# Kernel optimization log

Hardware: AMD Instinct MI355X
Metric: run time of the kernel (lower is better)

Reference implementation:

```python
import jax, jax.numpy as jnp
import numpy as np

EMBED_DIM = 1024
NUM_HEADS = 16
HEAD_DIM = EMBED_DIM // NUM_HEADS
FF_DIM = 4096
EPS = 1e-5


def layer_norm(x, gamma, beta):
    mu = jnp.mean(x, axis=-1, keepdims=True)
    var = jnp.var(x, axis=-1, keepdims=True)
    return (x - mu) * jax.lax.rsqrt(var + EPS) * gamma + beta


def setup_inputs() -> dict:
    key = jax.random.key(0)
    ks = jax.random.split(key, 10)
    B, S = 2, 2048
    sd = 1.0 / np.sqrt(EMBED_DIM)
    sf = 1.0 / np.sqrt(FF_DIM)
    return {
        "x": jax.random.normal(ks[0], (B, S, EMBED_DIM), jnp.float32),
        # grouped QKV: 3*num_heads groups, each embed_dim -> head_dim
        "Wqkv": jax.random.normal(ks[1], (3 * NUM_HEADS, EMBED_DIM, HEAD_DIM), jnp.float32) * sd,
        "bqkv": jnp.zeros((3 * NUM_HEADS, HEAD_DIM), jnp.float32),
        "Wo": jax.random.normal(ks[2], (EMBED_DIM, EMBED_DIM), jnp.float32) * sd,
        "bo": jnp.zeros((EMBED_DIM,), jnp.float32),
        "W1": jax.random.normal(ks[3], (EMBED_DIM, FF_DIM), jnp.float32) * sd,
        "b1": jnp.zeros((FF_DIM,), jnp.float32),
        "W2": jax.random.normal(ks[4], (FF_DIM, EMBED_DIM), jnp.float32) * sf,
        "b2": jnp.zeros((EMBED_DIM,), jnp.float32),
        "ln1_g": jnp.ones((EMBED_DIM,), jnp.float32),
        "ln1_b": jnp.zeros((EMBED_DIM,), jnp.float32),
        "ln2_g": jnp.ones((EMBED_DIM,), jnp.float32),
        "ln2_b": jnp.zeros((EMBED_DIM,), jnp.float32),
    }


def reference(x, Wqkv, bqkv, Wo, bo, W1, b1, W2, b2, ln1_g, ln1_b, ln2_g, ln2_b):
    B, S, D = x.shape
    normed = layer_norm(x, ln1_g, ln1_b)
    # grouped QKV projection: group g gets its own (D, head_dim) weight
    qkv = jnp.einsum('bsd,gdh->bgsh', normed, Wqkv) + bqkv[None, :, None, :]
    qkv = qkv.reshape(B, 3, NUM_HEADS, S, HEAD_DIM)
    q, k, v = qkv[:, 0], qkv[:, 1], qkv[:, 2]  # each [B, H, S, hd]
    attn = jnp.einsum('bhqd,bhkd->bhqk', q, k) / np.sqrt(HEAD_DIM)
    attn = jax.nn.softmax(attn, axis=-1)
    out = jnp.einsum('bhqk,bhkd->bhqd', attn, v)
    out = out.transpose(0, 2, 1, 3).reshape(B, S, D)
    out = out @ Wo + bo
    x = x + out
    normed2 = layer_norm(x, ln2_g, ln2_b)
    ff = jax.nn.relu(normed2 @ W1 + b1) @ W2 + b2
    return x + ff
```

## Files before the change

kernel.cpp:

```cpp
#include <hip/hip_runtime.h>
#include <stdint.h>

#define SEQ    2048
#define NB     2
#define NHEADS 16
#define HDIM   64
#define EMBED  1024
#define NROWS  (NB*SEQ)
#define QKVSZ  ((size_t)NB*NHEADS*SEQ*HDIM)

typedef __attribute__((ext_vector_type(8))) short short8;
typedef __attribute__((ext_vector_type(4))) float float4v;
typedef __attribute__((ext_vector_type(16))) float float16v;
typedef __attribute__((ext_vector_type(2))) unsigned int uint2v;
typedef __attribute__((ext_vector_type(4))) unsigned int uint4v;

__device__ __forceinline__ float b2f(unsigned short h) {
    unsigned int u = ((unsigned int)h) << 16;
    union { unsigned int u; float f; } c; c.u = u; return c.f;
}
__device__ __forceinline__ unsigned short f2b(float f) {
    union { float f; unsigned int u; } c; c.f = f;
    unsigned int u = c.u;
    u += 0x7FFFu + ((u >> 16) & 1u);
    return (unsigned short)(u >> 16);
}
__device__ __forceinline__ unsigned int fbits(float f) {
    union { float f; unsigned int u; } c; c.f = f; return c.u;
}
__device__ __forceinline__ unsigned int cvtpk_bf16(float lo, float hi) {
    unsigned int r;
    asm("v_cvt_pk_bf16_f32 %0, %1, %2" : "=v"(r) : "v"(lo), "v"(hi));
    return r;
}

__device__ __forceinline__ void gload_lds16(const void* g, void* l) {
    __builtin_amdgcn_global_load_lds(
        (const __attribute__((address_space(1))) unsigned int*)g,
        (__attribute__((address_space(3))) unsigned int*)l, 16, 0, 0);
}

__device__ __forceinline__ int probe_f32(const void* probe) {
    return ((const unsigned short*)probe)[0] == 0;
}
__device__ __forceinline__ float lde(const void* base, size_t off, int f32) {
    return f32 ? ((const float*)base)[off] : b2f(((const unsigned short*)base)[off]);
}
__device__ __forceinline__ void ste(void* base, size_t off, float v, int f32) {
    if (f32) ((float*)base)[off] = v;
    else     ((unsigned short*)base)[off] = f2b(v);
}

__global__ __launch_bounds__(256) void ln_kernel(
    const void* __restrict__ x,
    const void* __restrict__ g,
    const void* __restrict__ b,
    unsigned short* __restrict__ out,
    const void* __restrict__ probe)
{
    int f32 = probe_f32(probe);
    int row = blockIdx.x;
    int t = threadIdx.x;
    float v0, v1, v2, v3;
    if (f32) {
        float4 rv = ((const float4*)x)[(size_t)row * (EMBED / 4) + t];
        v0 = rv.x; v1 = rv.y; v2 = rv.z; v3 = rv.w;
    } else {
        ushort4 rv = ((const ushort4*)((const unsigned short*)x + (size_t)row * EMBED))[t];
        v0 = b2f(rv.x); v1 = b2f(rv.y); v2 = b2f(rv.z); v3 = b2f(rv.w);
    }
    float s  = v0 + v1 + v2 + v3;
    float sq = v0*v0 + v1*v1 + v2*v2 + v3*v3;
    #pragma unroll
    for (int off = 32; off > 0; off >>= 1) {
        s  += __shfl_xor(s,  off);
        sq += __shfl_xor(sq, off);
    }
    __shared__ float red[8];
    int lane = t & 63, wv = t >> 6;
    if (lane == 0) { red[wv] = s; red[wv + 4] = sq; }
    __syncthreads();
    s  = red[0] + red[1] + red[2] + red[3];
    sq = red[4] + red[5] + red[6] + red[7];
    float mu  = s * (1.0f / EMBED);
    float var = sq * (1.0f / EMBED) - mu * mu;
    float rs  = rsqrtf(var + 1e-5f);
    float g0 = lde(g, t*4+0, f32), g1 = lde(g, t*4+1, f32);
    float g2 = lde(g, t*4+2, f32), g3 = lde(g, t*4+3, f32);
    float b0 = lde(b, t*4+0, f32), b1 = lde(b, t*4+1, f32);
    float b2 = lde(b, t*4+2, f32), b3 = lde(b, t*4+3, f32);
    ushort4 ov;
    ov.x = f2b((v0 - mu) * rs * g0 + b0);
    ov.y = f2b((v1 - mu) * rs * g1 + b1);
    ov.z = f2b((v2 - mu) * rs * g2 + b2);
    ov.w = f2b((v3 - mu) * rs * g3 + b3);
    ((ushort4*)(out + (size_t)row * EMBED))[t] = ov;
}

template<int QKV>
__global__ __launch_bounds__(256) void transpose_kernel(
    const void* __restrict__ in,
    unsigned short* __restrict__ out, int K, int N,
    const void* __restrict__ probe)
{
    __shared__ unsigned short t[64 * 68];
    int f32 = probe_f32(probe);
    int tid = threadIdx.x;
    int n0 = blockIdx.x * 64, k0 = blockIdx.y * 64;
    #pragma unroll
    for (int i = 0; i < 4; i++) {
        int id = tid + i * 256;
        int kr = id >> 4, nc = (id & 15) * 4;
        size_t srcoff;
        if (QKV) srcoff = ((size_t)(n0 >> 6) << 16) + (size_t)(k0 + kr) * 64 + nc;
        else     srcoff = (size_t)(k0 + kr) * N + n0 + nc;
        ushort4 val;
        if (f32) {
            float4 rv = *(const float4*)((const float*)in + srcoff);
            val.x = f2b(rv.x); val.y = f2b(rv.y); val.z = f2b(rv.z); val.w = f2b(rv.w);
        } else {
            val = *(const ushort4*)((const unsigned short*)in + srcoff);
        }
        *(ushort4*)&t[kr * 68 + nc] = val;
    }
    __syncthreads();
    #pragma unroll
    for (int i = 0; i < 4; i++) {
        int id = tid + i * 256;
        int nr = id >> 4, kc = (id & 15) * 4;
        ushort4 o;
        o.x = t[(kc + 0) * 68 + nr];
        o.y = t[(kc + 1) * 68 + nr];
        o.z = t[(kc + 2) * 68 + nr];
        o.w = t[(kc + 3) * 68 + nr];
        *(ushort4*)(out + (size_t)(n0 + nr) * K + k0 + kc) = o;
    }
}

template<int DO_RELU, int HAS_BIAS, int OUTMODE>
__global__ __launch_bounds__(512) void gemm256_kernel(
    const unsigned short* __restrict__ A,
    const unsigned short* __restrict__ Bt,
    const void* __restrict__ bias,
    void* __restrict__ out,
    int M, int N, int Kloc, int ldA, int ldB,
    const void* __restrict__ probe)
{
    __shared__ unsigned short Als[2][256 * 64];
    __shared__ unsigned short Bls[2][256 * 64];
    int f32 = probe_f32(probe);
    int tid = threadIdx.x;
    int lane = tid & 63, wv = tid >> 6;
    int lq = lane >> 4, lr = lane & 15;
    int wr = wv >> 2, wc = wv & 3;
    int m0 = blockIdx.y * 256, n0 = blockIdx.x * 256;
    int k0 = blockIdx.z * Kloc;

    int srow = tid >> 3;
    int sch  = (tid & 7) ^ (srow & 7);
    const unsigned short* ga = A  + (size_t)(m0 + srow) * ldA + k0 + sch * 8;
    const unsigned short* gb = Bt + (size_t)(n0 + srow) * ldB + k0 + sch * 8;
    int ldst = tid * 8;
    int rx = lr & 7;

    float4v acc[8][4];
    #pragma unroll
    for (int i = 0; i < 8; i++)
        #pragma unroll
        for (int j = 0; j < 4; j++)
            { acc[i][j][0] = 0.f; acc[i][j][1] = 0.f; acc[i][j][2] = 0.f; acc[i][j][3] = 0.f; }

    int nkt = Kloc >> 6;
    #pragma unroll
    for (int u = 0; u < 4; u++)
        gload_lds16(ga + (size_t)u * 64 * ldA, &Als[0][u * 4096 + ldst]);
    #pragma unroll
    for (int u = 0; u < 4; u++)
        gload_lds16(gb + (size_t)u * 64 * ldB, &Bls[0][u * 4096 + ldst]);

    for (int kt = 0; kt < nkt; kt++) {
        int cur = kt & 1, nxt = cur ^ 1;
        if (kt + 1 < nkt) {
            int ko = (kt + 1) * 64;
            #pragma unroll
            for (int u = 0; u < 4; u++)
                gload_lds16(ga + (size_t)u * 64 * ldA + ko, &Als[nxt][u * 4096 + ldst]);
            asm volatile("s_waitcnt vmcnt(4)" ::: "memory");
        } else {
            asm volatile("s_waitcnt vmcnt(0)" ::: "memory");
        }
        __builtin_amdgcn_s_barrier();
        asm volatile("" ::: "memory");
        {
            short8 af[8], bf[4];
            #pragma unroll
            for (int mt = 0; mt < 8; mt++)
                af[mt] = *(const short8*)(
                    &Als[cur][(wr * 128 + mt * 16 + lr) * 64 + ((lq ^ rx) * 8)]);
            #pragma unroll
            for (int nt = 0; nt < 4; nt++)
                bf[nt] = *(const short8*)(
                    &Bls[cur][(wc * 64 + nt * 16 + lr) * 64 + ((lq ^ rx) * 8)]);
            __builtin_amdgcn_s_setprio(1);
            #pragma unroll
            for (int mt = 0; mt < 8; mt++)
                #pragma unroll
                for (int nt = 0; nt < 4; nt++)
                    acc[mt][nt] = __builtin_amdgcn_mfma_f32_16x16x32_bf16(af[mt], bf[nt], acc[mt][nt], 0, 0, 0);
            __builtin_amdgcn_s_setprio(0);
        }
        if (kt + 1 < nkt) {
            int ko = (kt + 1) * 64;
            #pragma unroll
            for (int u = 0; u < 4; u++)
                gload_lds16(gb + (size_t)u * 64 * ldB + ko, &Bls[nxt][u * 4096 + ldst]);
        }
        {
            short8 af[8], bf[4];
            #pragma unroll
            for (int mt = 0; mt < 8; mt++)
                af[mt] = *(const short8*)(
                    &Als[cur][(wr * 128 + mt * 16 + lr) * 64 + (((4 + lq) ^ rx) * 8)]);
            #pragma unroll
            for (int nt = 0; nt < 4; nt++)
                bf[nt] = *(const short8*)(
                    &Bls[cur][(wc * 64 + nt * 16 + lr) * 64 + (((4 + lq) ^ rx) * 8)]);
            __builtin_amdgcn_s_setprio(1);
            #pragma unroll
            for (int mt = 0; mt < 8; mt++)
                #pragma unroll
                for (int nt = 0; nt < 4; nt++)
                    acc[mt][nt] = __builtin_amdgcn_mfma_f32_16x16x32_bf16(af[mt], bf[nt], acc[mt][nt], 0, 0, 0);
            __builtin_amdgcn_s_setprio(0);
        }
        asm volatile("s_waitcnt lgkmcnt(0)" ::: "memory");
        __builtin_amdgcn_s_barrier();
    }

    if (OUTMODE == 3) {
        float* po = (float*)out + (size_t)blockIdx.z * M * N;
        #pragma unroll
        for (int mt = 0; mt < 8; mt++)
            #pragma unroll
            for (int nt = 0; nt < 4; nt++)
                #pragma unroll
                for (int rg = 0; rg < 4; rg++) {
                    int rr = m0 + wr * 128 + mt * 16 + lq * 4 + rg;
                    int cc = n0 + wc * 64 + nt * 16 + lr;
                    po[(size_t)rr * N + cc] = acc[mt][nt][rg];
                }
    } else if (OUTMODE == 2) {
        #pragma unroll
        for (int mt = 0; mt < 8; mt++) {
            int rrb = m0 + wr * 128 + mt * 16 + lq * 4;
            int bb = rrb >> 11, ss = rrb & 2047;
            #pragma unroll
            for (int nt = 0; nt < 4; nt++) {
                int cc = n0 + wc * 64 + nt * 16 + lr;
                int gg = cc >> 6, hd = cc & 63;
                int ty = gg >> 4, hh = gg & 15;
                float vv[4];
                #pragma unroll
                for (int rg = 0; rg < 4; rg++) {
                    float v = acc[mt][nt][rg];
                    if (HAS_BIAS) v += lde(bias, (size_t)cc, f32);
                    vv[rg] = v;
                }
                if (ty < 2) {
                    unsigned short* p = (unsigned short*)out + (size_t)ty * QKVSZ +
                        (((size_t)(bb * NHEADS + hh) * SEQ + ss) * HDIM) + hd;
                    #pragma unroll
                    for (int rg = 0; rg < 4; rg++) p[(size_t)rg * HDIM] = f2b(vv[rg]);
                } else {
                    ushort4 pk;
                    pk.x = f2b(vv[0]); pk.y = f2b(vv[1]);
                    pk.z = f2b(vv[2]); pk.w = f2b(vv[3]);
                    *(ushort4*)((unsigned short*)out + 2 * QKVSZ +
                        ((size_t)(bb * NHEADS + hh) * HDIM + hd) * SEQ + ss) = pk;
                }
            }
        }
    } else {
        #pragma unroll
        for (int mt = 0; mt < 8; mt++)
            #pragma unroll
            for (int nt = 0; nt < 4; nt++)
                #pragma unroll
                for (int rg = 0; rg < 4; rg++) {
                    int rr = m0 + wr * 128 + mt * 16 + lq * 4 + rg;
                    int cc = n0 + wc * 64 + nt * 16 + lr;
                    float v = acc[mt][nt][rg];
                    if (HAS_BIAS) v += lde(bias, (size_t)cc, f32);
                    if (DO_RELU) v = v > 0.f ? v : 0.f;
                    ((unsigned short*)out)[(size_t)rr * N + cc] = f2b(v);
                }
    }
}

template<int DO_RELU, int HAS_BIAS, int OUTMODE>
__global__ __launch_bounds__(512) void gemm256p8_kernel(
    const unsigned short* __restrict__ A,
    const unsigned short* __restrict__ Bt,
    const void* __restrict__ bias,
    void* __restrict__ out,
    int M, int N, int Kloc, int ldA, int ldB,
    const void* __restrict__ probe)
{
    __shared__ unsigned short Als[2][2][128 * 64];
    __shared__ unsigned short Bls[2][2][128 * 64];
    int f32 = probe_f32(probe);
    int tid = threadIdx.x;
    int lane = tid & 63, wv = tid >> 6;
    int lq = lane >> 4, lr = lane & 15;
    int wr = wv >> 2, wc = wv & 3;
    int m0 = blockIdx.y * 256, n0 = blockIdx.x * 256;
    int k0 = blockIdx.z * Kloc;

    int srow = tid >> 3;
    int sch  = (tid & 7) ^ (srow & 7);
    const unsigned short* ga = A  + (size_t)(m0 + srow) * ldA + k0 + sch * 8;
    const unsigned short* gb = Bt + (size_t)(n0 + srow) * ldB + k0 + sch * 8;
    int ldst = tid * 8;
    int rx = lr & 7;

    auto stA = [&](int d, int h, int ko) {
        gload_lds16(ga + (size_t)(h * 128) * ldA + ko, &Als[d][h][ldst]);
        gload_lds16(ga + (size_t)(h * 128 + 64) * ldA + ko, &Als[d][h][4096 + ldst]);
    };
    auto stB = [&](int d, int h, int ko) {
        gload_lds16(gb + (size_t)(h * 128) * ldB + ko, &Bls[d][h][ldst]);
        gload_lds16(gb + (size_t)(h * 128 + 64) * ldB + ko, &Bls[d][h][4096 + ldst]);
    };
    auto rdA = [&](int d, int qm, short8 (&af)[4][2]) {
        #pragma unroll
        for (int mt = 0; mt < 4; mt++)
            #pragma unroll
            for (int c = 0; c < 2; c++)
                af[mt][c] = *(const short8*)(&Als[d][qm][
                    (wr * 64 + mt * 16 + lr) * 64 + (((c * 4 + lq) ^ rx) * 8)]);
    };
    auto rdB = [&](int d, int qn, short8 (&bf)[2][2]) {
        #pragma unroll
        for (int nt = 0; nt < 2; nt++)
            #pragma unroll
            for (int c = 0; c < 2; c++)
                bf[nt][c] = *(const short8*)(&Bls[d][qn][
                    (wc * 32 + nt * 16 + lr) * 64 + (((c * 4 + lq) ^ rx) * 8)]);
    };
    auto MM = [&](short8 (&af)[4][2], short8 (&bf)[2][2], float4v (&aq)[4][2]) {
        __builtin_amdgcn_s_setprio(1);
        #pragma unroll
        for (int c = 0; c < 2; c++)
            #pragma unroll
            for (int mt = 0; mt < 4; mt++)
                #pragma unroll
                for (int nt = 0; nt < 2; nt++)
                    aq[mt][nt] = __builtin_amdgcn_mfma_f32_16x16x32_bf16(
                        af[mt][c], bf[nt][c], aq[mt][nt], 0, 0, 0);
        __builtin_amdgcn_s_setprio(0);
    };
    #define VMC(n)  asm volatile("s_waitcnt vmcnt(" #n ")" ::: "memory")
    #define BARF()  do { __builtin_amdgcn_s_barrier(); \
                         asm volatile("" ::: "memory"); } while (0)

    float4v acc00[4][2], acc01[4][2], acc11[4][2], acc10[4][2];
    #pragma unroll
    for (int i = 0; i < 4; i++)
        #pragma unroll
        for (int j = 0; j < 2; j++) {
            acc00[i][j] = float4v{0.f, 0.f, 0.f, 0.f};
            acc01[i][j] = float4v{0.f, 0.f, 0.f, 0.f};
            acc11[i][j] = float4v{0.f, 0.f, 0.f, 0.f};
            acc10[i][j] = float4v{0.f, 0.f, 0.f, 0.f};
        }
    short8 af0[4][2], af1[4][2], bf0[2][2], bf1[2][2];

    int nkt = Kloc >> 6;
    int npair = nkt >> 1;

    stA(0, 0, 0); stB(0, 0, 0); stB(0, 1, 0); stA(0, 1, 0);
    VMC(4); BARF();
    rdA(0, 0, af0); rdB(0, 0, bf0);

    for (int p = 0; p < npair - 1; p++) {
        int koB  = (2 * p + 1) * 64;
        int koA2 = (2 * p + 2) * 64;
        MM(af0, bf0, acc00); stA(1, 0, koB); VMC(4); BARF(); rdB(0, 1, bf1);
        MM(af0, bf1, acc01); stB(1, 0, koB); VMC(4); BARF(); rdA(0, 1, af1);
        MM(af1, bf1, acc11); stB(1, 1, koB);         BARF(); rdB(0, 0, bf0);
        MM(af1, bf0, acc10); stA(1, 1, koB); VMC(4); BARF(); rdA(1, 0, af0); rdB(1, 0, bf1);
        MM(af0, bf1, acc00); stA(0, 0, koA2); VMC(4); BARF(); rdB(1, 1, bf0);
        MM(af0, bf0, acc01); stB(0, 0, koA2); VMC(4); BARF(); rdA(1, 1, af1);
        MM(af1, bf0, acc11); stB(0, 1, koA2);         BARF(); rdB(1, 0, bf1);
        MM(af1, bf1, acc10); stA(0, 1, koA2); VMC(4); BARF(); rdA(0, 0, af0); rdB(0, 0, bf0);
    }
    {
        int koB = (nkt - 1) * 64;
        MM(af0, bf0, acc00); stA(1, 0, koB); VMC(4); BARF(); rdB(0, 1, bf1);
        MM(af0, bf1, acc01); stB(1, 0, koB); VMC(4); BARF(); rdA(0, 1, af1);
        MM(af1, bf1, acc11); stB(1, 1, koB);         BARF(); rdB(0, 0, bf0);
        MM(af1, bf0, acc10); stA(1, 1, koB); VMC(4); BARF(); rdA(1, 0, af0); rdB(1, 0, bf1);
        MM(af0, bf1, acc00);                  VMC(2); BARF(); rdB(1, 1, bf0);
        MM(af0, bf0, acc01);                  VMC(0); BARF(); rdA(1, 1, af1);
        MM(af1, bf0, acc11);                          BARF(); rdB(1, 0, bf1);
        MM(af1, bf1, acc10);
    }
    #undef VMC
    #undef BARF

    auto storeQ = [&](int qr, int qc, float4v (&aq)[4][2]) {
        if (OUTMODE == 3) {
            float* po = (float*)out + (size_t)blockIdx.z * M * N;
            #pragma unroll
            for (int mt = 0; mt < 4; mt++)
                #pragma unroll
                for (int nt = 0; nt < 2; nt++)
                    #pragma unroll
                    for (int rg = 0; rg < 4; rg++) {
                        int rr = m0 + qr * 128 + wr * 64 + mt * 16 + lq * 4 + rg;
                        int cc = n0 + qc * 128 + wc * 32 + nt * 16 + lr;
                        po[(size_t)rr * N + cc] = aq[mt][nt][rg];
                    }
        } else {
            #pragma unroll
            for (int mt = 0; mt < 4; mt++)
                #pragma unroll
                for (int nt = 0; nt < 2; nt++)
                    #pragma unroll
                    for (int rg = 0; rg < 4; rg++) {
                        int rr = m0 + qr * 128 + wr * 64 + mt * 16 + lq * 4 + rg;
                        int cc = n0 + qc * 128 + wc * 32 + nt * 16 + lr;
                        float v = aq[mt][nt][rg];
                        if (HAS_BIAS) v += lde(bias, (size_t)cc, f32);
                        if (DO_RELU) v = v > 0.f ? v : 0.f;
                        ((unsigned short*)out)[(size_t)rr * N + cc] = f2b(v);
                    }
        }
    };
    storeQ(0, 0, acc00); storeQ(0, 1, acc01);
    storeQ(1, 1, acc11); storeQ(1, 0, acc10);
}

__global__ __launch_bounds__(256) void ff2_combine_kernel(
    const float* __restrict__ part,
    const void* __restrict__ b2,
    void* __restrict__ xout,
    const void* __restrict__ probe)
{
    int f32 = probe_f32(probe);
    int row = blockIdx.x;
    int t = threadIdx.x;
    const size_t MN = (size_t)NROWS * EMBED;
    size_t base = (size_t)row * EMBED + t * 4;
    float4 p0 = *(const float4*)(part + base);
    float4 p1 = *(const float4*)(part + MN + base);
    float4 p2 = *(const float4*)(part + 2 * MN + base);
    float4 p3 = *(const float4*)(part + 3 * MN + base);
    float s0 = (p0.x + p1.x) + (p2.x + p3.x);
    float s1 = (p0.y + p1.y) + (p2.y + p3.y);
    float s2 = (p0.z + p1.z) + (p2.z + p3.z);
    float s3 = (p0.w + p1.w) + (p2.w + p3.w);
    int c = t * 4;
    s0 += lde(b2, c + 0, f32) + lde(xout, base + 0, f32);
    s1 += lde(b2, c + 1, f32) + lde(xout, base + 1, f32);
    s2 += lde(b2, c + 2, f32) + lde(xout, base + 2, f32);
    s3 += lde(b2, c + 3, f32) + lde(xout, base + 3, f32);
    ste(xout, base + 0, s0, f32);
    ste(xout, base + 1, s1, f32);
    ste(xout, base + 2, s2, f32);
    ste(xout, base + 3, s3, f32);
}

template<int DO_RELU, int HAS_BIAS, int HAS_RES, int OUTMODE>
__global__ __launch_bounds__(256) void gemm64_kernel(
    const unsigned short* __restrict__ A,
    const unsigned short* __restrict__ Bt,
    const void* __restrict__ bias,
    const void* __restrict__ res,
    void* __restrict__ out,
    int M, int N, int K, int ldA, int ldB,
    const void* __restrict__ probe)
{
    __shared__ unsigned short Als[2][64 * 32];
    __shared__ unsigned short Bls[2][64 * 32];
    int f32 = probe_f32(probe);
    int tid = threadIdx.x;
    int lane = tid & 63, wv = tid >> 6;
    int lq = lane >> 4, lr = lane & 15;
    int moff = (wv >> 1) * 32, noff = (wv & 1) * 32;
    int m0 = blockIdx.y * 64, n0 = blockIdx.x * 64;

    int rA = tid >> 2, jA = tid & 3;
    int jjA = jA ^ ((rA >> 1) & 3);
    const unsigned short* ga = A  + (size_t)(m0 + rA) * ldA + jjA * 8;
    const unsigned short* gb = Bt + (size_t)(n0 + rA) * ldB + jjA * 8;

    int fch = (lq ^ ((lr >> 1) & 3)) * 8;

    float4v acc[2][2];
    #pragma unroll
    for (int i = 0; i < 2; i++)
        #pragma unroll
        for (int j = 0; j < 2; j++)
            { acc[i][j][0] = 0.f; acc[i][j][1] = 0.f; acc[i][j][2] = 0.f; acc[i][j][3] = 0.f; }

    gload_lds16(ga, &Als[0][(size_t)tid * 8]);
    gload_lds16(gb, &Bls[0][(size_t)tid * 8]);

    int nkt = K >> 5;
    for (int kt = 0; kt < nkt; kt++) {
        int cur = kt & 1, nxt = cur ^ 1;
        __syncthreads();
        if (kt + 1 < nkt) {
            int ko = (kt + 1) * 32;
            gload_lds16(ga + ko, &Als[nxt][(size_t)tid * 8]);
            gload_lds16(gb + ko, &Bls[nxt][(size_t)tid * 8]);
        }
        short8 af[2], bfr[2];
        #pragma unroll
        for (int mt = 0; mt < 2; mt++)
            af[mt] = *(const short8*)(&Als[cur][(moff + mt * 16 + lr) * 32 + fch]);
        #pragma unroll
        for (int nt = 0; nt < 2; nt++)
            bfr[nt] = *(const short8*)(&Bls[cur][(noff + nt * 16 + lr) * 32 + fch]);
        #pragma unroll
        for (int mt = 0; mt < 2; mt++)
            #pragma unroll
            for (int nt = 0; nt < 2; nt++)
                acc[mt][nt] = __builtin_amdgcn_mfma_f32_16x16x32_bf16(af[mt], bfr[nt], acc[mt][nt], 0, 0, 0);
    }

    #pragma unroll
    for (int mt = 0; mt < 2; mt++) {
        #pragma unroll
        for (int nt = 0; nt < 2; nt++) {
            #pragma unroll
            for (int rg = 0; rg < 4; rg++) {
                int rr = m0 + moff + mt * 16 + lq * 4 + rg;
                int cc = n0 + noff + nt * 16 + lr;
                float v = acc[mt][nt][rg];
                if (HAS_BIAS) v += lde(bias, (size_t)cc, f32);
                if (DO_RELU) v = v > 0.f ? v : 0.f;
                if (HAS_RES) v += lde(res, (size_t)rr * N + cc, f32);
                if (OUTMODE == 1) ste(out, (size_t)rr * N + cc, v, f32);
                else ((unsigned short*)out)[(size_t)rr * N + cc] = f2b(v);
            }
        }
    }
}

__global__ __launch_bounds__(256) void attn_kernel(
    const unsigned short* __restrict__ qb,
    const unsigned short* __restrict__ kb,
    const unsigned short* __restrict__ vtb,
    unsigned short* __restrict__ outb)
{
    __shared__ unsigned short Kls[3][64 * 64];
    __shared__ unsigned short Vls[3][64 * 64];
    int tid = threadIdx.x;
    int lane = tid & 63, wv = tid >> 6;
    int l31 = lane & 31, hh = lane >> 5;
    int bh = blockIdx.y;
    int b = bh >> 4, head = bh & 15;
    const unsigned short* q  = qb  + (size_t)bh * SEQ * HDIM;
    const unsigned short* k  = kb  + (size_t)bh * SEQ * HDIM;
    const unsigned short* vt = vtb + (size_t)bh * HDIM * SEQ;
    int q0w = blockIdx.x * 128 + wv * 32;

    const float C2 = 0.18033688011112042f;

    short8 qf[4];
    #pragma unroll
    for (int c = 0; c < 4; c++) {
        short8 raw = *(const short8*)(q + (size_t)(q0w + l31) * HDIM + c * 16 + hh * 8);
        #pragma unroll
        for (int j = 0; j < 8; j++)
            qf[c][j] = (short)f2b(b2f((unsigned short)raw[j]) * C2);
    }

    int rS = tid >> 3;
    int jjS = (tid & 7) ^ (rS & 7);
    const unsigned short* gk0 = k + (size_t)rS * HDIM + jjS * 8;
    const unsigned short* gk1 = k + (size_t)(rS + 32) * HDIM + jjS * 8;
    const unsigned short* gv0 = vt + (size_t)rS * SEQ + jjS * 8;
    const unsigned short* gv1 = vt + (size_t)(rS + 32) * SEQ + jjS * 8;

    float l_part = 0.f;
    float16v o0, o1;
    #pragma unroll
    for (int i = 0; i < 16; i++) { o0[i] = 0.f; o1[i] = 0.f; }

    auto stage = [&](int bf, int kt) {
        int k0n = kt * 64;
        gload_lds16(gk0 + (size_t)k0n * HDIM, &Kls[bf][(size_t)tid * 8]);
        gload_lds16(gk1 + (size_t)k0n * HDIM, &Kls[bf][(size_t)(tid + 256) * 8]);
        gload_lds16(gv0 + k0n, &Vls[bf][(size_t)tid * 8]);
        gload_lds16(gv1 + k0n, &Vls[bf][(size_t)(tid + 256) * 8]);
    };

    const int NT = SEQ / 64;
    stage(0, 0);
    stage(1, 1);

    int cur = 0;
    for (int kt = 0; kt < NT; kt++) {
        if (kt + 1 < NT) asm volatile("s_waitcnt vmcnt(4)" ::: "memory");
        else             asm volatile("s_waitcnt vmcnt(0)" ::: "memory");
        __builtin_amdgcn_s_barrier();
        asm volatile("" ::: "memory");
        if (kt + 2 < NT) {
            int nb = cur + 2; if (nb >= 3) nb -= 3;
            stage(nb, kt + 2);
        }

        float16v st0, st1;
        #pragma unroll
        for (int i = 0; i < 16; i++) { st0[i] = 0.f; st1[i] = 0.f; }
        {
            int r0 = l31, r1 = 32 + l31;
            int rxk = l31 & 7;
            __builtin_amdgcn_s_setprio(1);
            #pragma unroll
            for (int c = 0; c < 4; c++) {
                short8 kf0 = *(const short8*)(
                    &Kls[cur][r0 * 64 + (((2 * c + hh) ^ rxk) * 8)]);
                st0 = __builtin_amdgcn_mfma_f32_32x32x16_bf16(kf0, qf[c], st0, 0, 0, 0);
                short8 kf1 = *(const short8*)(
                    &Kls[cur][r1 * 64 + (((2 * c + hh) ^ rxk) * 8)]);
                st1 = __builtin_amdgcn_mfma_f32_32x32x16_bf16(kf1, qf[c], st1, 0, 0, 0);
            }
            __builtin_amdgcn_s_setprio(0);
        }

        int rv0 = l31, rv1 = 32 + l31;
        int rxv = l31 & 7;
        #pragma unroll
        for (int kb2 = 0; kb2 < 2; kb2++) {
            float p[16];
            #pragma unroll
            for (int rg = 0; rg < 16; rg++) {
                float sv = kb2 ? st1[rg] : st0[rg];
                p[rg] = __builtin_amdgcn_exp2f(sv);
                l_part += p[rg];
            }
            #pragma unroll
            for (int s = 0; s < 2; s++) {
                unsigned int a1 = cvtpk_bf16(p[8*s+0], p[8*s+1]);
                unsigned int a2 = cvtpk_bf16(p[8*s+2], p[8*s+3]);
                unsigned int b1 = cvtpk_bf16(p[8*s+4], p[8*s+5]);
                unsigned int b2 = cvtpk_bf16(p[8*s+6], p[8*s+7]);
                uint2v r1 = __builtin_amdgcn_permlane32_swap(a1, b1, false, false);
                uint2v r2 = __builtin_amdgcn_permlane32_swap(a2, b2, false, false);
                union { uint4v u; short8 s8; } pun;
                pun.u.x = r1.x; pun.u.y = r2.x; pun.u.z = r1.y; pun.u.w = r2.y;
                short8 pf = pun.s8;
                int g = kb2 * 2 + s;
                short8 vf0 = *(const short8*)(
                    &Vls[cur][rv0 * 64 + (((2 * g + hh) ^ rxv) * 8)]);
                short8 vf1 = *(const short8*)(
                    &Vls[cur][rv1 * 64 + (((2 * g + hh) ^ rxv) * 8)]);
                __builtin_amdgcn_s_setprio(1);
                o0 = __builtin_amdgcn_mfma_f32_32x32x16_bf16(pf, vf0, o0, 0, 0, 0);
                o1 = __builtin_amdgcn_mfma_f32_32x32x16_bf16(pf, vf1, o1, 0, 0, 0);
                __builtin_amdgcn_s_setprio(0);
            }
        }
        cur = cur + 1; if (cur >= 3) cur -= 3;
    }

    l_part += __shfl_xor(l_part, 32);
    float linv_me = 1.f / l_part;
    #pragma unroll
    for (int rg = 0; rg < 16; rg++) {
        int qrow = (rg & 3) + 8 * (rg >> 2) + 4 * hh;
        float linv = __shfl(linv_me, qrow);
        size_t rowbase = ((size_t)(b * SEQ + q0w + qrow)) * EMBED + head * HDIM;
        outb[rowbase + l31]      = f2b(o0[rg] * linv);
        outb[rowbase + 32 + l31] = f2b(o1[rg] * linv);
    }
}

extern "C" void kernel_launch(void* const* d_in, const int* in_sizes, int n_in,
                              void* d_out, int out_size, void* d_ws, size_t ws_size,
                              hipStream_t stream)
{
    (void)in_sizes; (void)n_in; (void)out_size;
    const void* x    = d_in[0];
    const void* Wqkv = d_in[1];
    const void* bqkv = d_in[2];
    const void* Wo   = d_in[3];
    const void* bo   = d_in[4];
    const void* W1   = d_in[5];
    const void* b1   = d_in[6];
    const void* W2   = d_in[7];
    const void* b2   = d_in[8];
    const void* g1   = d_in[9];
    const void* be1  = d_in[10];
    const void* g2   = d_in[11];
    const void* be2  = d_in[12];
    const void* probe = g1;

    char* ws = (char*)d_ws;
    const size_t MB = 1024 * 1024;
    unsigned short* tmp1  = (unsigned short*)(ws + 0 * MB);
    unsigned short* qkv   = (unsigned short*)(ws + 8 * MB);
    unsigned short* WoT   = (unsigned short*)(ws + 8 * MB);
    unsigned short* W1T   = (unsigned short*)(ws + 8 * MB);
    unsigned short* W2T   = (unsigned short*)(ws + 8 * MB);
    unsigned short* h1    = (unsigned short*)(ws + 16 * MB);
    float*          part  = (float*)(ws + 48 * MB);
    unsigned short* WqkvT = (unsigned short*)d_out;
    bool splitk_ok = ws_size >= (size_t)112 * MB;

    transpose_kernel<1><<<dim3(3072 / 64, 1024 / 64), 256, 0, stream>>>(Wqkv, WqkvT, 1024, 3072, probe);
    ln_kernel<<<dim3(NROWS), 256, 0, stream>>>(x, g1, be1, tmp1, probe);
    gemm256_kernel<0, 1, 2><<<dim3(3072 / 256, NROWS / 256), 512, 0, stream>>>(
        tmp1, WqkvT, bqkv, qkv, NROWS, 3072, 1024, 1024, 1024, probe);
    attn_kernel<<<dim3(SEQ / 128, NB * NHEADS), 256, 0, stream>>>(
        qkv, qkv + QKVSZ, qkv + 2 * QKVSZ, tmp1);
    transpose_kernel<0><<<dim3(1024 / 64, 1024 / 64), 256, 0, stream>>>(Wo, WoT, 1024, 1024, probe);
    gemm64_kernel<0, 1, 1, 1><<<dim3(1024 / 64, NROWS / 64), 256, 0, stream>>>(
        tmp1, WoT, bo, x, d_out, NROWS, 1024, 1024, 1024, 1024, probe);
    ln_kernel<<<dim3(NROWS), 256, 0, stream>>>(d_out, g2, be2, tmp1, probe);
    transpose_kernel<0><<<dim3(4096 / 64, 1024 / 64), 256, 0, stream>>>(W1, W1T, 1024, 4096, probe);
    gemm256p8_kernel<1, 1, 0><<<dim3(4096 / 256, NROWS / 256), 512, 0, stream>>>(
        tmp1, W1T, b1, h1, NROWS, 4096, 1024, 1024, 1024, probe);
    transpose_kernel<0><<<dim3(1024 / 64, 4096 / 64), 256, 0, stream>>>(W2, W2T, 4096, 1024, probe);
    if (splitk_ok) {
        gemm256p8_kernel<0, 0, 3><<<dim3(1024 / 256, NROWS / 256, 4), 512, 0, stream>>>(
            h1, W2T, nullptr, part, NROWS, 1024, 1024, 4096, 4096, probe);
        ff2_combine_kernel<<<dim3(NROWS), 256, 0, stream>>>(part, b2, d_out, probe);
    } else {
        gemm64_kernel<0, 1, 1, 1><<<dim3(1024 / 64, NROWS / 64), 256, 0, stream>>>(
            h1, W2T, b2, d_out, d_out, NROWS, 1024, 4096, 4096, 4096, probe);
    }
}
```

Measured before the change: 386.5 us.

## Split attention KV range across two wave groups and combine partials via LDS

```diff
diff --git a/kernel.cpp b/kernel.cpp
--- a/kernel.cpp
+++ b/kernel.cpp
@@ -549,23 +549,24 @@
     }
 }
 
-__global__ __launch_bounds__(256) void attn_kernel(
+__global__ __launch_bounds__(512) void attn_kernel(
     const unsigned short* __restrict__ qb,
     const unsigned short* __restrict__ kb,
     const unsigned short* __restrict__ vtb,
     unsigned short* __restrict__ outb)
 {
-    __shared__ unsigned short Kls[3][64 * 64];
-    __shared__ unsigned short Vls[3][64 * 64];
+    __shared__ unsigned short Kls[2][2][64 * 64];
+    __shared__ unsigned short Vls[2][2][64 * 64];
     int tid = threadIdx.x;
     int lane = tid & 63, wv = tid >> 6;
     int l31 = lane & 31, hh = lane >> 5;
+    int qg = wv & 3, half = wv >> 2;
     int bh = blockIdx.y;
     int b = bh >> 4, head = bh & 15;
     const unsigned short* q  = qb  + (size_t)bh * SEQ * HDIM;
     const unsigned short* k  = kb  + (size_t)bh * SEQ * HDIM;
     const unsigned short* vt = vtb + (size_t)bh * HDIM * SEQ;
-    int q0w = blockIdx.x * 128 + wv * 32;
+    int q0w = blockIdx.x * 128 + qg * 32;
 
     const float C2 = 0.18033688011112042f;
 
@@ -578,40 +579,43 @@
             qf[c][j] = (short)f2b(b2f((unsigned short)raw[j]) * C2);
     }
 
-    int rS = tid >> 3;
-    int jjS = (tid & 7) ^ (rS & 7);
+    int ts = tid & 255;
+    int rS = ts >> 3;
+    int jjS = (ts & 7) ^ (rS & 7);
+    const int NTH = SEQ / 128;
+    int tbase = half * NTH;
     const unsigned short* gk0 = k + (size_t)rS * HDIM + jjS * 8;
     const unsigned short* gk1 = k + (size_t)(rS + 32) * HDIM + jjS * 8;
     const unsigned short* gv0 = vt + (size_t)rS * SEQ + jjS * 8;
     const unsigned short* gv1 = vt + (size_t)(rS + 32) * SEQ + jjS * 8;
 
+    auto stage = [&](int bf, int tl) {
+        int k0n = (tbase + tl) * 64;
+        gload_lds16(gk0 + (size_t)k0n * HDIM, &Kls[half][bf][(size_t)ts * 8]);
+        gload_lds16(gk1 + (size_t)k0n * HDIM, &Kls[half][bf][(size_t)(ts + 256) * 8]);
+        gload_lds16(gv0 + k0n, &Vls[half][bf][(size_t)ts * 8]);
+        gload_lds16(gv1 + k0n, &Vls[half][bf][(size_t)(ts + 256) * 8]);
+    };
+
     float l_part = 0.f;
     float16v o0, o1;
     #pragma unroll
     for (int i = 0; i < 16; i++) { o0[i] = 0.f; o1[i] = 0.f; }
 
-    auto stage = [&](int bf, int kt) {
-        int k0n = kt * 64;
-        gload_lds16(gk0 + (size_t)k0n * HDIM, &Kls[bf][(size_t)tid * 8]);
-        gload_lds16(gk1 + (size_t)k0n * HDIM, &Kls[bf][(size_t)(tid + 256) * 8]);
-        gload_lds16(gv0 + k0n, &Vls[bf][(size_t)tid * 8]);
-        gload_lds16(gv1 + k0n, &Vls[bf][(size_t)(tid + 256) * 8]);
-    };
-
-    const int NT = SEQ / 64;
     stage(0, 0);
-    stage(1, 1);
-
-    int cur = 0;
-    for (int kt = 0; kt < NT; kt++) {
-        if (kt + 1 < NT) asm volatile("s_waitcnt vmcnt(4)" ::: "memory");
-        else             asm volatile("s_waitcnt vmcnt(0)" ::: "memory");
+
+    for (int t = 0; t < NTH; t++) {
+        int cur = t & 1;
         __builtin_amdgcn_s_barrier();
         asm volatile("" ::: "memory");
-        if (kt + 2 < NT) {
-            int nb = cur + 2; if (nb >= 3) nb -= 3;
-            stage(nb, kt + 2);
-        }
+        if (t + 1 < NTH) {
+            stage(cur ^ 1, t + 1);
+            asm volatile("s_waitcnt vmcnt(4)" ::: "memory");
+        } else {
+            asm volatile("s_waitcnt vmcnt(0)" ::: "memory");
+        }
+        __builtin_amdgcn_s_barrier();
+        asm volatile("" ::: "memory");
 
         float16v st0, st1;
         #pragma unroll
@@ -623,10 +627,10 @@
             #pragma unroll
             for (int c = 0; c < 4; c++) {
                 short8 kf0 = *(const short8*)(
-                    &Kls[cur][r0 * 64 + (((2 * c + hh) ^ rxk) * 8)]);
+                    &Kls[half][cur][r0 * 64 + (((2 * c + hh) ^ rxk) * 8)]);
                 st0 = __builtin_amdgcn_mfma_f32_32x32x16_bf16(kf0, qf[c], st0, 0, 0, 0);
                 short8 kf1 = *(const short8*)(
-                    &Kls[cur][r1 * 64 + (((2 * c + hh) ^ rxk) * 8)]);
+                    &Kls[half][cur][r1 * 64 + (((2 * c + hh) ^ rxk) * 8)]);
                 st1 = __builtin_amdgcn_mfma_f32_32x32x16_bf16(kf1, qf[c], st1, 0, 0, 0);
             }
             __builtin_amdgcn_s_setprio(0);
@@ -656,27 +660,60 @@
                 short8 pf = pun.s8;
                 int g = kb2 * 2 + s;
                 short8 vf0 = *(const short8*)(
-                    &Vls[cur][rv0 * 64 + (((2 * g + hh) ^ rxv) * 8)]);
+                    &Vls[half][cur][rv0 * 64 + (((2 * g + hh) ^ rxv) * 8)]);
                 short8 vf1 = *(const short8*)(
-                    &Vls[cur][rv1 * 64 + (((2 * g + hh) ^ rxv) * 8)]);
+                    &Vls[half][cur][rv1 * 64 + (((2 * g + hh) ^ rxv) * 8)]);
                 __builtin_amdgcn_s_setprio(1);
                 o0 = __builtin_amdgcn_mfma_f32_32x32x16_bf16(pf, vf0, o0, 0, 0, 0);
                 o1 = __builtin_amdgcn_mfma_f32_32x32x16_bf16(pf, vf1, o1, 0, 0, 0);
                 __builtin_amdgcn_s_setprio(0);
             }
         }
-        cur = cur + 1; if (cur >= 3) cur -= 3;
     }
 
     l_part += __shfl_xor(l_part, 32);
-    float linv_me = 1.f / l_part;
-    #pragma unroll
-    for (int rg = 0; rg < 16; rg++) {
-        int qrow = (rg & 3) + 8 * (rg >> 2) + 4 * hh;
-        float linv = __shfl(linv_me, qrow);
-        size_t rowbase = ((size_t)(b * SEQ + q0w + qrow)) * EMBED + head * HDIM;
-        outb[rowbase + l31]      = f2b(o0[rg] * linv);
-        outb[rowbase + 32 + l31] = f2b(o1[rg] * linv);
+
+    __syncthreads();
+    float* obuf = (float*)&Kls[0][0][0];
+    float* lbuf = (float*)&Vls[0][0][0];
+    if (half == 1) {
+        float* od = obuf + (size_t)qg * 2048 + lane * 4;
+        #pragma unroll
+        for (int ib = 0; ib < 4; ib++) {
+            float4 v4;
+            v4.x = o0[ib*4+0]; v4.y = o0[ib*4+1]; v4.z = o0[ib*4+2]; v4.w = o0[ib*4+3];
+            *(float4*)(od + ib * 256) = v4;
+        }
+        #pragma unroll
+        for (int ib = 0; ib < 4; ib++) {
+            float4 v4;
+            v4.x = o1[ib*4+0]; v4.y = o1[ib*4+1]; v4.z = o1[ib*4+2]; v4.w = o1[ib*4+3];
+            *(float4*)(od + (ib + 4) * 256) = v4;
+        }
+        if (hh == 0) lbuf[qg * 32 + l31] = l_part;
+    }
+    __syncthreads();
+    if (half == 0) {
+        float* od = obuf + (size_t)qg * 2048 + lane * 4;
+        #pragma unroll
+        for (int ib = 0; ib < 4; ib++) {
+            float4 v4 = *(const float4*)(od + ib * 256);
+            o0[ib*4+0] += v4.x; o0[ib*4+1] += v4.y; o0[ib*4+2] += v4.z; o0[ib*4+3] += v4.w;
+        }
+        #pragma unroll
+        for (int ib = 0; ib < 4; ib++) {
+            float4 v4 = *(const float4*)(od + (ib + 4) * 256);
+            o1[ib*4+0] += v4.x; o1[ib*4+1] += v4.y; o1[ib*4+2] += v4.z; o1[ib*4+3] += v4.w;
+        }
+        float linv_me = 1.f / (l_part + lbuf[qg * 32 + l31]);
+        #pragma unroll
+        for (int rg = 0; rg < 16; rg++) {
+            int qrow = (rg & 3) + 8 * (rg >> 2) + 4 * hh;
+            float linv = __shfl(linv_me, qrow);
+            size_t rowbase = ((size_t)(b * SEQ + q0w + qrow)) * EMBED + head * HDIM;
+            outb[rowbase + l31]      = f2b(o0[rg] * linv);
+            outb[rowbase + 32 + l31] = f2b(o1[rg] * linv);
+        }
     }
 }
 
@@ -716,7 +753,7 @@
     ln_kernel<<<dim3(NROWS), 256, 0, stream>>>(x, g1, be1, tmp1, probe);
     gemm256_kernel<0, 1, 2><<<dim3(3072 / 256, NROWS / 256), 512, 0, stream>>>(
         tmp1, WqkvT, bqkv, qkv, NROWS, 3072, 1024, 1024, 1024, probe);
-    attn_kernel<<<dim3(SEQ / 128, NB * NHEADS), 256, 0, stream>>>(
+    attn_kernel<<<dim3(SEQ / 128, NB * NHEADS), 512, 0, stream>>>(
         qkv, qkv + QKVSZ, qkv + 2 * QKVSZ, tmp1);
     transpose_kernel<0><<<dim3(1024 / 64, 1024 / 64), 256, 0, stream>>>(Wo, WoT, 1024, 1024, probe);
     gemm64_kernel<0, 1, 1, 1><<<dim3(1024 / 64, NROWS / 64), 256, 0, stream>>>(
```

Result: faster. 370.0 us (-4.3%).
